# Optimization experiments

Hardware: AMD Instinct MI355X
Metric: run time of the kernel (lower is better)

Reference implementation:

```python
import jax, jax.numpy as jnp
import numpy as np

B, D = 8192, 1024          # batch, input dim
UNITS = [1024, 512]        # expert MLP hidden sizes
T, E_T, E_S = 2, 2, 4      # num_tasks, experts per task, shared experts
E = T * E_T + E_S          # total experts = 8


def setup_inputs() -> dict:
    key = jax.random.key(0)
    k = jax.random.split(key, 6)
    H, O = UNITS
    x = jax.random.normal(k[0], (B, D), dtype=jnp.float32)
    # glorot-normal-ish scaling for expert weights
    W1 = jax.random.normal(k[1], (E, D, H), dtype=jnp.float32) * np.sqrt(2.0 / (D + H))
    b1 = jnp.zeros((E, H), dtype=jnp.float32)
    W2 = jax.random.normal(k[2], (E, H, O), dtype=jnp.float32) * np.sqrt(2.0 / (H + O))
    b2 = jnp.zeros((E, O), dtype=jnp.float32)
    # per-task gate over (E_T + E_S) experts, no bias (use_bias=False in Dense)
    Wg = jax.random.normal(k[3], (T, D, E_T + E_S), dtype=jnp.float32) * np.sqrt(2.0 / (D + E_T + E_S))
    # shared gate over all E experts
    Wgs = jax.random.normal(k[4], (D, E), dtype=jnp.float32) * np.sqrt(2.0 / (D + E))
    return {"x": x, "W1": W1, "b1": b1, "W2": W2, "b2": b2, "Wg": Wg, "Wgs": Wgs}


def reference(x, W1, b1, W2, b2, Wg, Wgs):
    # All experts see the same input (2D-input path of CGC3: tf.tile over experts).
    # Batched grouped GEMM over the expert axis instead of a Python loop.
    h = jax.nn.relu(jnp.einsum('bd,edh->ebh', x, W1) + b1[:, None, :])   # [E,B,H]
    eo = jax.nn.relu(jnp.einsum('ebh,eho->ebo', h, W2) + b2[:, None, :]) # [E,B,O]

    outs = []
    for i in range(T):
        # experts for task i = its own E_T experts + the last E_S shared experts
        idx = jnp.array(list(range(i * E_T, (i + 1) * E_T)) + list(range(E - E_S, E)))
        g = jax.nn.softmax(x @ Wg[i], axis=-1)            # [B, E_T+E_S]
        sel = eo[idx]                                     # [E_T+E_S, B, O]
        outs.append(jnp.einsum('be,ebo->bo', g, sel))     # [B, O]
    # output_share=True: share tower gated over all experts
    gs = jax.nn.softmax(x @ Wgs, axis=-1)                 # [B, E]
    outs.append(jnp.einsum('be,ebo->bo', gs, eo))         # [B, O]
    return jnp.stack(outs, axis=1)                        # [B, T+1, O]
```

## Files before the change

### kernel.cpp

```cpp
#include <hip/hip_runtime.h>
#include <hip/hip_bf16.h>
#include <stdint.h>

#define B_SZ 8192
#define D_SZ 1024
#define H_SZ 1024
#define O_SZ 512
#define E_SZ 8

typedef float f32x4 __attribute__((ext_vector_type(4)));
typedef __bf16 bf16x8 __attribute__((ext_vector_type(8)));

typedef __attribute__((address_space(1))) uint32_t gu32;
typedef __attribute__((address_space(3))) uint32_t lu32;

__device__ __forceinline__ unsigned short f2bf(float f) {
    union { __hip_bfloat16 h; unsigned short u; } c;
    c.h = __float2bfloat16(f);
    return c.u;
}
__device__ __forceinline__ float bf2f(unsigned short u) {
    union { float f; uint32_t u; } c;
    c.u = ((uint32_t)u) << 16;
    return c.f;
}

__global__ __launch_bounds__(256) void k_convert(const float* __restrict__ in,
                                                 unsigned short* __restrict__ out, int n8) {
    int i = blockIdx.x * 256 + threadIdx.x;
    if (i >= n8) return;
    const float4* p = (const float4*)in + (size_t)i * 2;
    float4 a = p[0], b = p[1];
    ushort4 lo, hi;
    lo.x = f2bf(a.x); lo.y = f2bf(a.y); lo.z = f2bf(a.z); lo.w = f2bf(a.w);
    hi.x = f2bf(b.x); hi.y = f2bf(b.y); hi.z = f2bf(b.z); hi.w = f2bf(b.w);
    ushort4* q = (ushort4*)out + (size_t)i * 2;
    q[0] = lo; q[1] = hi;
}

__global__ __launch_bounds__(256) void k_transpose_convert(const float* __restrict__ in,
                                                           unsigned short* __restrict__ out,
                                                           int R, int C) {
    __shared__ float tile[32][33];
    const float* src = in + (size_t)blockIdx.z * R * C;
    unsigned short* dst = out + (size_t)blockIdx.z * R * C;
    int c0 = blockIdx.x * 32, r0 = blockIdx.y * 32;
    int tx = threadIdx.x, ty = threadIdx.y;
#pragma unroll
    for (int rr = ty; rr < 32; rr += 8)
        tile[rr][tx] = src[(size_t)(r0 + rr) * C + c0 + tx];
    __syncthreads();
#pragma unroll
    for (int rr = ty; rr < 32; rr += 8)
        dst[(size_t)(c0 + rr) * R + r0 + tx] = f2bf(tile[tx][rr]);
}

__global__ __launch_bounds__(256) void k_gates(const float* __restrict__ x,
                                               const float* __restrict__ Wg,
                                               const float* __restrict__ Wgs,
                                               float* __restrict__ g_all) {
    const int wv = threadIdx.x >> 6;
    const int lane = threadIdx.x & 63;
    const int b = blockIdx.x * 4 + wv;
    const float* xr = x + (size_t)b * D_SZ;
    float acc[20];
#pragma unroll
    for (int j = 0; j < 20; ++j) acc[j] = 0.f;
    for (int d = lane; d < D_SZ; d += 64) {
        float xv = xr[d];
        const float* w0 = Wg + (size_t)d * 6;
        const float* w1 = Wg + (size_t)D_SZ * 6 + (size_t)d * 6;
        const float* ws = Wgs + (size_t)d * 8;
#pragma unroll
        for (int j = 0; j < 6; ++j) acc[j] += xv * w0[j];
#pragma unroll
        for (int j = 0; j < 6; ++j) acc[6 + j] += xv * w1[j];
#pragma unroll
        for (int j = 0; j < 8; ++j) acc[12 + j] += xv * ws[j];
    }
#pragma unroll
    for (int j = 0; j < 20; ++j) {
        float v = acc[j];
#pragma unroll
        for (int s = 32; s > 0; s >>= 1) v += __shfl_down(v, s, 64);
        acc[j] = v;
    }
    if (lane == 0) {
        float* g = g_all + (size_t)b * 20;
#pragma unroll
        for (int t = 0; t < 3; ++t) {
            int base = (t == 0) ? 0 : (t == 1 ? 6 : 12);
            int cnt  = (t == 2) ? 8 : 6;
            float m = -1e30f;
            for (int j = 0; j < cnt; ++j) m = fmaxf(m, acc[base + j]);
            float ex[8]; float sum = 0.f;
            for (int j = 0; j < cnt; ++j) { ex[j] = __expf(acc[base + j] - m); sum += ex[j]; }
            float inv = 1.f / sum;
            for (int j = 0; j < cnt; ++j) g[base + j] = ex[j] * inv;
        }
    }
}

__global__ __launch_bounds__(512, 2) void k_gemm4(
    const unsigned short* __restrict__ A,
    const unsigned short* __restrict__ Bt,
    const float* __restrict__ bias,
    unsigned short* __restrict__ C,
    int M, int N, int K,
    long long sA, long long sB, long long sBias, long long sC, int e_base) {

    const int tid = threadIdx.x;
    const int lane = tid & 63, wid = tid >> 6;
    const int wr = wid >> 2, wc = wid & 3;
    const int lr = lane & 15, lg = lane >> 4;

    const int nwg = gridDim.x;
    const int wg = blockIdx.x;
    const int swz = (wg & 7) * (nwg >> 3) + (wg >> 3);
    const int nx = N >> 8;
    const int my = M >> 8;
    const int bx = swz % nx;
    const int t1 = swz / nx;
    const int by = t1 % my;
    const int e  = t1 / my + e_base;

    A    += (size_t)((long long)e * sA);
    Bt   += (size_t)((long long)e * sB);
    bias += (size_t)((long long)e * sBias);
    C    += (size_t)((long long)e * sC);

    const int m0 = by * 256, n0 = bx * 256;

    __shared__ __align__(16) unsigned short lds[65536];
    char* ldsb = (char*)lds;

    const int srow = tid >> 2;
    const int scol = (((tid & 3) ^ ((tid >> 3) & 3)) * 8);
    const int sdst = tid * 16;

    auto stageA = [&](int t) {
        const int bb = (t & 3) * 32768;
        const unsigned short* s0 = A + (size_t)(m0 + srow) * K + (t << 5) + scol;
        __builtin_amdgcn_global_load_lds((gu32*)s0, (lu32*)(ldsb + bb + sdst), 16, 0, 0);
        __builtin_amdgcn_global_load_lds((gu32*)(s0 + (size_t)128 * K),
                                         (lu32*)(ldsb + bb + 8192 + sdst), 16, 0, 0);
    };
    auto stageB = [&](int t) {
        const int bb = (t & 3) * 32768 + 16384;
        const unsigned short* s0 = Bt + (size_t)(n0 + srow) * K + (t << 5) + scol;
        __builtin_amdgcn_global_load_lds((gu32*)s0, (lu32*)(ldsb + bb + sdst), 16, 0, 0);
        __builtin_amdgcn_global_load_lds((gu32*)(s0 + (size_t)128 * K),
                                         (lu32*)(ldsb + bb + 8192 + sdst), 16, 0, 0);
    };

    const int cblk = (lg ^ ((lr >> 1) & 3)) * 16;
    const int aoff = wr * 8192 + lr * 64 + cblk;
    const int boff = 16384 + (wc >> 1) * 8192 + (wc & 1) * 4096 + lr * 64 + cblk;

    f32x4 acc[8][4];
#pragma unroll
    for (int i = 0; i < 8; ++i)
#pragma unroll
        for (int j = 0; j < 4; ++j)
            acc[i][j] = f32x4{0.f, 0.f, 0.f, 0.f};

    const int NT = K >> 5;

    stageA(0); stageB(0); stageA(1); stageB(1); stageA(2); stageB(2);
    asm volatile("s_waitcnt vmcnt(8)" ::: "memory");
    asm volatile("s_barrier" ::: "memory");

    for (int t = 0; t < NT; ++t) {
        const int bb = (t & 3) * 32768;

        bf16x8 bq[4], af[4];
#pragma unroll
        for (int j = 0; j < 4; ++j)
            bq[j] = *(const bf16x8*)(ldsb + bb + boff + j * 1024);
#pragma unroll
        for (int i = 0; i < 4; ++i)
            af[i] = *(const bf16x8*)(ldsb + bb + aoff + i * 1024);
        if (t + 3 < NT) stageA(t + 3);
        asm volatile("s_barrier" ::: "memory");
        __builtin_amdgcn_s_setprio(1);
#pragma unroll
        for (int i = 0; i < 4; ++i)
#pragma unroll
            for (int j = 0; j < 4; ++j)
                acc[i][j] = __builtin_amdgcn_mfma_f32_16x16x32_bf16(af[i], bq[j], acc[i][j], 0, 0, 0);
        __builtin_amdgcn_s_setprio(0);
        asm volatile("s_barrier" ::: "memory");

        bf16x8 ag[4];
#pragma unroll
        for (int i = 0; i < 4; ++i)
            ag[i] = *(const bf16x8*)(ldsb + bb + aoff + (4 + i) * 1024);
        if (t + 3 < NT) stageB(t + 3);
        asm volatile("s_barrier" ::: "memory");
        __builtin_amdgcn_s_setprio(1);
#pragma unroll
        for (int i = 0; i < 4; ++i)
#pragma unroll
            for (int j = 0; j < 4; ++j)
                acc[4 + i][j] = __builtin_amdgcn_mfma_f32_16x16x32_bf16(ag[i], bq[j], acc[4 + i][j], 0, 0, 0);
        __builtin_amdgcn_s_setprio(0);
        if (t < NT - 3)       { asm volatile("s_waitcnt vmcnt(8)" ::: "memory"); }
        else if (t == NT - 3) { asm volatile("s_waitcnt vmcnt(4)" ::: "memory"); }
        else if (t == NT - 2) { asm volatile("s_waitcnt vmcnt(0)" ::: "memory"); }
        asm volatile("s_barrier" ::: "memory");
    }

#pragma unroll
    for (int j = 0; j < 4; ++j) {
        const int n = n0 + wc * 64 + j * 16 + lr;
        const float bv = bias[n];
#pragma unroll
        for (int i = 0; i < 8; ++i) {
            const int mb = m0 + wr * 128 + i * 16 + lg * 4;
#pragma unroll
            for (int r = 0; r < 4; ++r) {
                float v = fmaxf(acc[i][j][r] + bv, 0.f);
                C[(size_t)(mb + r) * N + n] = f2bf(v);
            }
        }
    }
}

__global__ __launch_bounds__(256) void k_combine(const unsigned short* __restrict__ eo,
                                                 const float* __restrict__ g_all,
                                                 float* __restrict__ out) {
    int idx = blockIdx.x * 256 + threadIdx.x;
    int b = idx >> 9;
    int o = idx & 511;
    const float* g = g_all + (size_t)b * 20;
    float v[E_SZ];
#pragma unroll
    for (int e = 0; e < E_SZ; ++e)
        v[e] = bf2f(eo[(size_t)e * (B_SZ * (size_t)O_SZ) + idx]);
    float o0 = g[0] * v[0] + g[1] * v[1] + g[2] * v[4] + g[3] * v[5] + g[4] * v[6] + g[5] * v[7];
    float o1 = g[6] * v[2] + g[7] * v[3] + g[8] * v[4] + g[9] * v[5] + g[10] * v[6] + g[11] * v[7];
    float o2 = 0.f;
#pragma unroll
    for (int e = 0; e < E_SZ; ++e) o2 += g[12 + e] * v[e];
    size_t ob = (size_t)b * (3 * O_SZ) + o;
    out[ob] = o0;
    out[ob + O_SZ] = o1;
    out[ob + 2 * O_SZ] = o2;
}

extern "C" void kernel_launch(void* const* d_in, const int* in_sizes, int n_in,
                              void* d_out, int out_size, void* d_ws, size_t ws_size,
                              hipStream_t stream) {
    const float* x   = (const float*)d_in[0];
    const float* W1  = (const float*)d_in[1];
    const float* b1  = (const float*)d_in[2];
    const float* W2  = (const float*)d_in[3];
    const float* b2  = (const float*)d_in[4];
    const float* Wg  = (const float*)d_in[5];
    const float* Wgs = (const float*)d_in[6];
    float* out = (float*)d_out;

    char* ws = (char*)d_ws;
    const size_t SZ_XBF  = (size_t)B_SZ * D_SZ * 2;
    const size_t SZ_W1T  = (size_t)E_SZ * H_SZ * D_SZ * 2;
    const size_t SZ_W2T  = (size_t)E_SZ * O_SZ * H_SZ * 2;
    const size_t SZ_EO   = (size_t)E_SZ * B_SZ * O_SZ * 2;
    const size_t SZ_G    = (size_t)B_SZ * 20 * 4;
    const size_t SZ_HBIG = (size_t)E_SZ * B_SZ * H_SZ * 2;

    unsigned short* x_bf = (unsigned short*)ws;              ws += SZ_XBF;
    unsigned short* W1T  = (unsigned short*)ws;              ws += SZ_W1T;
    unsigned short* W2T  = (unsigned short*)ws;              ws += SZ_W2T;
    unsigned short* eo   = (unsigned short*)ws;              ws += SZ_EO;
    float* g_all         = (float*)ws;                       ws += SZ_G;
    unsigned short* h_buf = (unsigned short*)ws;

    const size_t fixed = SZ_XBF + SZ_W1T + SZ_W2T + SZ_EO + SZ_G;
    const bool big = ws_size >= fixed + SZ_HBIG;

    k_convert<<<(B_SZ * D_SZ / 8 + 255) / 256, 256, 0, stream>>>(x, x_bf, B_SZ * D_SZ / 8);
    dim3 tb(32, 8);
    k_transpose_convert<<<dim3(H_SZ / 32, D_SZ / 32, E_SZ), tb, 0, stream>>>(W1, W1T, D_SZ, H_SZ);
    k_transpose_convert<<<dim3(O_SZ / 32, H_SZ / 32, E_SZ), tb, 0, stream>>>(W2, W2T, H_SZ, O_SZ);

    k_gates<<<B_SZ / 4, 256, 0, stream>>>(x, Wg, Wgs, g_all);

    if (big) {
        k_gemm4<<<(H_SZ / 256) * (B_SZ / 256) * E_SZ, 512, 0, stream>>>(
            x_bf, W1T, b1, h_buf, B_SZ, H_SZ, D_SZ,
            0LL, (long long)H_SZ * D_SZ, (long long)H_SZ, (long long)B_SZ * H_SZ, 0);
        k_gemm4<<<(O_SZ / 256) * (B_SZ / 256) * E_SZ, 512, 0, stream>>>(
            h_buf, W2T, b2, eo, B_SZ, O_SZ, H_SZ,
            (long long)B_SZ * H_SZ, (long long)O_SZ * H_SZ, (long long)O_SZ, (long long)B_SZ * O_SZ, 0);
    } else {
        for (int e = 0; e < E_SZ; ++e) {
            k_gemm4<<<(H_SZ / 256) * (B_SZ / 256), 512, 0, stream>>>(
                x_bf, W1T, b1, h_buf, B_SZ, H_SZ, D_SZ,
                0LL, (long long)H_SZ * D_SZ, (long long)H_SZ, 0LL, e);
            k_gemm4<<<(O_SZ / 256) * (B_SZ / 256), 512, 0, stream>>>(
                h_buf, W2T, b2, eo, B_SZ, O_SZ, H_SZ,
                0LL, (long long)O_SZ * H_SZ, (long long)O_SZ, (long long)B_SZ * O_SZ, e);
        }
    }

    k_combine<<<(B_SZ * O_SZ) / 256, 256, 0, stream>>>(eo, g_all, out);
}
```

Baseline: 344.3 us.

## Stage GEMM epilogue through LDS, vectorize combine, enlarge transpose tiles

The GEMM epilogue now writes the bias+ReLU bf16 tile into LDS and then copies it out with coalesced 16-byte row stores, replacing scattered 2-byte global stores. The combine kernel processes four outputs per thread using ushort4 loads and float4 stores. The weight transpose uses 64x64 tiles with 512-thread blocks. Together these target global-memory store efficiency, at the cost of more LDS traffic and one extra barrier in the GEMM epilogue. The LDS staging assumes the existing shared buffer can hold the full 256x256 bf16 output tile.

Result: faster. 311.3 us (-9.6%).

```diff
diff --git a/kernel.cpp b/kernel.cpp
--- a/kernel.cpp
+++ b/kernel.cpp
@@ -38,20 +38,20 @@
     q[0] = lo; q[1] = hi;
 }
 
-__global__ __launch_bounds__(256) void k_transpose_convert(const float* __restrict__ in,
+__global__ __launch_bounds__(512) void k_transpose_convert(const float* __restrict__ in,
                                                            unsigned short* __restrict__ out,
                                                            int R, int C) {
-    __shared__ float tile[32][33];
+    __shared__ float tile[64][65];
     const float* src = in + (size_t)blockIdx.z * R * C;
     unsigned short* dst = out + (size_t)blockIdx.z * R * C;
-    int c0 = blockIdx.x * 32, r0 = blockIdx.y * 32;
+    int c0 = blockIdx.x * 64, r0 = blockIdx.y * 64;
     int tx = threadIdx.x, ty = threadIdx.y;
 #pragma unroll
-    for (int rr = ty; rr < 32; rr += 8)
+    for (int rr = ty; rr < 64; rr += 8)
         tile[rr][tx] = src[(size_t)(r0 + rr) * C + c0 + tx];
     __syncthreads();
 #pragma unroll
-    for (int rr = ty; rr < 32; rr += 8)
+    for (int rr = ty; rr < 64; rr += 8)
         dst[(size_t)(c0 + rr) * R + r0 + tx] = f2bf(tile[tx][rr]);
 }
 
@@ -210,42 +210,61 @@
         asm volatile("s_barrier" ::: "memory");
     }
 
+    unsigned short* ct = (unsigned short*)ldsb;
 #pragma unroll
     for (int j = 0; j < 4; ++j) {
-        const int n = n0 + wc * 64 + j * 16 + lr;
-        const float bv = bias[n];
+        const int nn = wc * 64 + j * 16 + lr;
+        const float bv = bias[n0 + nn];
 #pragma unroll
         for (int i = 0; i < 8; ++i) {
-            const int mb = m0 + wr * 128 + i * 16 + lg * 4;
+            const int mb = wr * 128 + i * 16 + lg * 4;
 #pragma unroll
             for (int r = 0; r < 4; ++r) {
                 float v = fmaxf(acc[i][j][r] + bv, 0.f);
-                C[(size_t)(mb + r) * N + n] = f2bf(v);
+                ct[(size_t)(mb + r) * 256 + nn] = f2bf(v);
             }
         }
+    }
+    __syncthreads();
+#pragma unroll
+    for (int it = 0; it < 16; ++it) {
+        const int row = it * 16 + (tid >> 5);
+        const int colE = (tid & 31) * 8;
+        *(int4*)(&C[(size_t)(m0 + row) * N + n0 + colE]) =
+            *(const int4*)(ldsb + it * 8192 + (size_t)tid * 16);
     }
 }
 
 __global__ __launch_bounds__(256) void k_combine(const unsigned short* __restrict__ eo,
                                                  const float* __restrict__ g_all,
                                                  float* __restrict__ out) {
-    int idx = blockIdx.x * 256 + threadIdx.x;
-    int b = idx >> 9;
-    int o = idx & 511;
+    int idx4 = blockIdx.x * 256 + threadIdx.x;
+    int b = idx4 >> 7;
+    int o4 = (idx4 & 127) * 4;
     const float* g = g_all + (size_t)b * 20;
-    float v[E_SZ];
-#pragma unroll
-    for (int e = 0; e < E_SZ; ++e)
-        v[e] = bf2f(eo[(size_t)e * (B_SZ * (size_t)O_SZ) + idx]);
-    float o0 = g[0] * v[0] + g[1] * v[1] + g[2] * v[4] + g[3] * v[5] + g[4] * v[6] + g[5] * v[7];
-    float o1 = g[6] * v[2] + g[7] * v[3] + g[8] * v[4] + g[9] * v[5] + g[10] * v[6] + g[11] * v[7];
-    float o2 = 0.f;
-#pragma unroll
-    for (int e = 0; e < E_SZ; ++e) o2 += g[12 + e] * v[e];
-    size_t ob = (size_t)b * (3 * O_SZ) + o;
-    out[ob] = o0;
-    out[ob + O_SZ] = o1;
-    out[ob + 2 * O_SZ] = o2;
+    float v[E_SZ][4];
+#pragma unroll
+    for (int e = 0; e < E_SZ; ++e) {
+        ushort4 u = *(const ushort4*)(eo + (size_t)e * B_SZ * O_SZ + (size_t)b * O_SZ + o4);
+        v[e][0] = bf2f(u.x); v[e][1] = bf2f(u.y); v[e][2] = bf2f(u.z); v[e][3] = bf2f(u.w);
+    }
+    float4 r0, r1, r2;
+    float* p0 = (float*)&r0; float* p1 = (float*)&r1; float* p2 = (float*)&r2;
+#pragma unroll
+    for (int c = 0; c < 4; ++c) {
+        p0[c] = g[0] * v[0][c] + g[1] * v[1][c] + g[2] * v[4][c] + g[3] * v[5][c]
+              + g[4] * v[6][c] + g[5] * v[7][c];
+        p1[c] = g[6] * v[2][c] + g[7] * v[3][c] + g[8] * v[4][c] + g[9] * v[5][c]
+              + g[10] * v[6][c] + g[11] * v[7][c];
+        float s = 0.f;
+#pragma unroll
+        for (int e = 0; e < E_SZ; ++e) s += g[12 + e] * v[e][c];
+        p2[c] = s;
+    }
+    size_t ob = (size_t)b * (3 * O_SZ) + o4;
+    *(float4*)(out + ob) = r0;
+    *(float4*)(out + ob + O_SZ) = r1;
+    *(float4*)(out + ob + 2 * O_SZ) = r2;
 }
 
 extern "C" void kernel_launch(void* const* d_in, const int* in_sizes, int n_in,
@@ -279,9 +298,9 @@
     const bool big = ws_size >= fixed + SZ_HBIG;
 
     k_convert<<<(B_SZ * D_SZ / 8 + 255) / 256, 256, 0, stream>>>(x, x_bf, B_SZ * D_SZ / 8);
-    dim3 tb(32, 8);
-    k_transpose_convert<<<dim3(H_SZ / 32, D_SZ / 32, E_SZ), tb, 0, stream>>>(W1, W1T, D_SZ, H_SZ);
-    k_transpose_convert<<<dim3(O_SZ / 32, H_SZ / 32, E_SZ), tb, 0, stream>>>(W2, W2T, H_SZ, O_SZ);
+    dim3 tb(64, 8);
+    k_transpose_convert<<<dim3(H_SZ / 64, D_SZ / 64, E_SZ), tb, 0, stream>>>(W1, W1T, D_SZ, H_SZ);
+    k_transpose_convert<<<dim3(O_SZ / 64, H_SZ / 64, E_SZ), tb, 0, stream>>>(W2, W2T, H_SZ, O_SZ);
 
     k_gates<<<B_SZ / 4, 256, 0, stream>>>(x, Wg, Wgs, g_all);
 
@@ -303,5 +322,5 @@
         }
     }
 
-    k_combine<<<(B_SZ * O_SZ) / 256, 256, 0, stream>>>(eo, g_all, out);
-}
+    k_combine<<<(B_SZ * O_SZ / 4) / 256, 256, 0, stream>>>(eo, g_all, out);
+}
```
